# Performance work log

Hardware: AMD Instinct MI355X
Metric: run time of the kernel (lower is better)

Reference implementation:

```python
import jax, jax.numpy as jnp
import numpy as np

B, NB, T, C, H, FW, TW = 4, 64, 512, 256, 8, 8, 8
HD = C // H
SCALE = HD ** -0.5
EPS = 1e-5


def setup_inputs() -> dict:
    key = jax.random.key(0)
    ks = jax.random.split(key, 12)
    inpt = jax.random.normal(ks[0], (B, NB, T, C), jnp.float32)
    perm_n = jax.vmap(lambda k: jax.random.permutation(k, NB))(jax.random.split(ks[1], B)).astype(jnp.int32)
    perm_t = jax.vmap(lambda k: jax.random.permutation(k, T))(jax.random.split(ks[2], B)).astype(jnp.int32)
    w = lambda k, shp: (jax.random.normal(k, shp, jnp.float32) * 0.02)
    return {
        "inpt": inpt, "perm_n": perm_n, "perm_t": perm_t,
        "ln_g": jnp.ones((C,), jnp.float32), "ln_b": jnp.zeros((C,), jnp.float32),
        "Wq": w(ks[3], (C, C)), "bq": jnp.zeros((C,), jnp.float32),
        "Wk": w(ks[4], (C, C)), "bk": jnp.zeros((C,), jnp.float32),
        "Wv": w(ks[5], (C, C)), "bv": jnp.zeros((C,), jnp.float32),
        "Wp": w(ks[6], (C, C)), "bp": jnp.zeros((C,), jnp.float32),
    }


def _layernorm(x, g, b):
    m = x.mean(-1, keepdims=True)
    v = ((x - m) ** 2).mean(-1, keepdims=True)
    return (x - m) * jax.lax.rsqrt(v + EPS) * g + b


def reference(inpt, perm_n, perm_t, ln_g, ln_b, Wq, bq, Wk, bk, Wv, bv, Wp, bp):
    x = _layernorm(inpt, ln_g, ln_b)  # (B, NB, T, C)

    # per-batch shuffle: gather along N then along T
    shuffled = jax.vmap(lambda xb, pn, pt: xb[pn][:, pt])(x, perm_n, perm_t)

    # window partition -> (B*NB/FW*T/TW, FW*TW, C)
    win = shuffled.reshape(B, NB // FW, FW, T // TW, TW, C)
    win = win.transpose(0, 1, 3, 2, 4, 5).reshape(-1, FW * TW, C)

    def heads(y):  # (Bw, L, C) -> (Bw, H, L, HD)
        return y.reshape(y.shape[0], y.shape[1], H, HD).transpose(0, 2, 1, 3)

    q = heads(win @ Wq.T + bq) * SCALE
    k = heads(win @ Wk.T + bk)
    v = heads(win @ Wv.T + bv)

    attn = jax.nn.softmax(jnp.einsum('bhqd,bhkd->bhqk', q, k), axis=-1)
    o = jnp.einsum('bhqk,bhkd->bhqd', attn, v)
    o = o.transpose(0, 2, 1, 3).reshape(-1, FW * TW, C)
    o = o @ Wp.T + bp

    # window reverse -> (B, NB, T, C)
    y = o.reshape(B, NB // FW, T // TW, FW, TW, C)
    y = y.transpose(0, 1, 3, 2, 4, 5).reshape(B, NB, T, C)

    # scatter reverse == gather with inverse permutations
    inv_n = jnp.argsort(perm_n, axis=-1)
    inv_t = jnp.argsort(perm_t, axis=-1)
    unshuf = jax.vmap(lambda yb, qn, qt: yb[:, qt][qn])(y, inv_n, inv_t)

    return inpt + unshuf
```

## Files before the change

kernel.cpp:

```cpp
#include <hip/hip_runtime.h>

typedef __attribute__((ext_vector_type(4))) float f32x4;
typedef __attribute__((ext_vector_type(8))) short bf16x8;

#define EPS_ 1e-5f
#define QSC 0.25503639409729144f

#define XS 264
#define SCB 16896
#define CHUNK 7424
#define QSTR 40
#define KOFF 2560
#define PSTR 72
#define VTOFF 5120
#define VSTR 72
#define LDS_US 76288
#define LDS_BYTES (LDS_US * 2 + 256)

__device__ __forceinline__ unsigned int pack2(float a, float b) {
  union { float f; unsigned int u; } ua, ub;
  ua.f = a; ub.f = b;
  unsigned int ra = (ua.u + 0x7FFFu + ((ua.u >> 16) & 1u)) >> 16;
  unsigned int rb = (ub.u + 0x7FFFu + ((ub.u >> 16) & 1u)) & 0xFFFF0000u;
  return ra | rb;
}
__device__ __forceinline__ uint2 pack4(f32x4 v) {
  uint2 o; o.x = pack2(v[0], v[1]); o.y = pack2(v[2], v[3]); return o;
}
__device__ __forceinline__ unsigned short f2b(float f) {
  union { float f; unsigned int u; } c; c.f = f;
  return (unsigned short)((c.u + 0x7FFFu + ((c.u >> 16) & 1u)) >> 16);
}

__global__ __launch_bounds__(256) void k0_cvt(const float* __restrict__ w0,
                                              const float* __restrict__ w1,
                                              const float* __restrict__ w2,
                                              const float* __restrict__ w3,
                                              unsigned short* __restrict__ dst) {
  int idx = blockIdx.x * 256 + threadIdx.x;
  const float* s = (blockIdx.y == 0) ? w0 : (blockIdx.y == 1) ? w1 : (blockIdx.y == 2) ? w2 : w3;
  dst[blockIdx.y * 65536 + idx] = f2b(s[idx]);
}

__global__ __launch_bounds__(512, 2) void ka_fused(
    const unsigned short* __restrict__ Wall,
    const float* __restrict__ ln_g, const float* __restrict__ ln_b,
    const int* __restrict__ pn, const int* __restrict__ pt,
    const float* __restrict__ bq, const float* __restrict__ bk,
    const float* __restrict__ bv, const float* __restrict__ bp,
    const float* __restrict__ inpt, float* __restrict__ out) {
  extern __shared__ unsigned short lds[];
  int* tok_off = (int*)(lds + LDS_US);

  const int tid = threadIdx.x;
  const int wv = tid >> 6, lane = tid & 63, quad = lane >> 4, l15 = lane & 15;
  const int w = blockIdx.x;
  const int b = w >> 9, nbb = (w >> 6) & 7, tbb = w & 63;
  const f32x4 z4 = {0.f, 0.f, 0.f, 0.f};

  if (tid < 64) {
    const int n = (nbb << 3) + (tid >> 3), t = (tbb << 3) + (tid & 7);
    tok_off[tid] = (((b << 6) + pn[(b << 6) + n]) * 512 + pt[(b << 9) + t]) * 256;
  }

  {
    const int n = (nbb << 3) + wv;
    const int spn = pn[(b << 6) + n];
    const float* rowbase = inpt + (size_t)((b << 6) + spn) * 512 * 256;
    const float4 gg = ((const float4*)ln_g)[lane];
    const float4 bb = ((const float4*)ln_b)[lane];
    float4 v[8];
    #pragma unroll
    for (int i = 0; i < 8; ++i) {
      const int spt = pt[(b << 9) + (tbb << 3) + i];
      v[i] = ((const float4*)(rowbase + (size_t)spt * 256))[lane];
    }
    #pragma unroll
    for (int i = 0; i < 8; ++i) {
      float s = v[i].x + v[i].y + v[i].z + v[i].w;
      float ss = v[i].x * v[i].x + v[i].y * v[i].y + v[i].z * v[i].z + v[i].w * v[i].w;
      #pragma unroll
      for (int m = 1; m < 64; m <<= 1) { s += __shfl_xor(s, m); ss += __shfl_xor(ss, m); }
      const float mean = s * (1.0f / 256.0f);
      const float rs = rsqrtf(ss * (1.0f / 256.0f) - mean * mean + EPS_);
      ushort4 o;
      o.x = f2b((v[i].x - mean) * rs * gg.x + bb.x);
      o.y = f2b((v[i].y - mean) * rs * gg.y + bb.y);
      o.z = f2b((v[i].z - mean) * rs * gg.z + bb.z);
      o.w = f2b((v[i].w - mean) * rs * gg.w + bb.w);
      ((ushort4*)(lds + (wv * 8 + i) * XS))[lane] = o;
    }
  }
  __syncthreads();

  const unsigned short* Wq = Wall;
  const unsigned short* Wk = Wall + 65536;
  const unsigned short* Wv_ = Wall + 131072;
  const unsigned short* Wp = Wall + 196608;
  unsigned short* chunk = lds + SCB + wv * CHUNK;
  const int h = wv;

  f32x4 qa[2][4], ka_[2][4], va[4][2];
  #pragma unroll
  for (int m2 = 0; m2 < 2; ++m2)
    #pragma unroll
    for (int nt = 0; nt < 4; ++nt) { qa[m2][nt] = z4; ka_[m2][nt] = z4; }
  #pragma unroll
  for (int mt = 0; mt < 4; ++mt)
    #pragma unroll
    for (int m2 = 0; m2 < 2; ++m2) va[mt][m2] = z4;

  #pragma unroll
  for (int ks = 0; ks < 8; ++ks) {
    bf16x8 bx[4];
    #pragma unroll
    for (int nt = 0; nt < 4; ++nt)
      bx[nt] = *(const bf16x8*)(lds + (nt * 16 + l15) * XS + ks * 32 + quad * 8);
    #pragma unroll
    for (int m2 = 0; m2 < 2; ++m2) {
      const int wrow = (h * 32 + m2 * 16 + l15) * 256 + ks * 32 + quad * 8;
      bf16x8 wq8 = *(const bf16x8*)(Wq + wrow);
      bf16x8 wk8 = *(const bf16x8*)(Wk + wrow);
      bf16x8 wv8 = *(const bf16x8*)(Wv_ + wrow);
      #pragma unroll
      for (int nt = 0; nt < 4; ++nt) {
        qa[m2][nt] = __builtin_amdgcn_mfma_f32_16x16x32_bf16(wq8, bx[nt], qa[m2][nt], 0, 0, 0);
        ka_[m2][nt] = __builtin_amdgcn_mfma_f32_16x16x32_bf16(wk8, bx[nt], ka_[m2][nt], 0, 0, 0);
        va[nt][m2] = __builtin_amdgcn_mfma_f32_16x16x32_bf16(bx[nt], wv8, va[nt][m2], 0, 0, 0);
      }
    }
  }

  #pragma unroll
  for (int m2 = 0; m2 < 2; ++m2) {
    float4 bq4 = ((const float4*)(bq + h * 32 + m2 * 16))[quad];
    float4 bk4 = ((const float4*)(bk + h * 32 + m2 * 16))[quad];
    #pragma unroll
    for (int nt = 0; nt < 4; ++nt) {
      f32x4 qv, kv;
      qv[0] = (qa[m2][nt][0] + bq4.x) * QSC; kv[0] = ka_[m2][nt][0] + bk4.x;
      qv[1] = (qa[m2][nt][1] + bq4.y) * QSC; kv[1] = ka_[m2][nt][1] + bk4.y;
      qv[2] = (qa[m2][nt][2] + bq4.z) * QSC; kv[2] = ka_[m2][nt][2] + bk4.z;
      qv[3] = (qa[m2][nt][3] + bq4.w) * QSC; kv[3] = ka_[m2][nt][3] + bk4.w;
      *(uint2*)(chunk + (nt * 16 + l15) * QSTR + m2 * 16 + quad * 4) = pack4(qv);
      *(uint2*)(chunk + KOFF + (nt * 16 + l15) * QSTR + m2 * 16 + quad * 4) = pack4(kv);
    }
    const float bvv = bv[h * 32 + m2 * 16 + l15];
    #pragma unroll
    for (int mt = 0; mt < 4; ++mt) {
      f32x4 vv;
      vv[0] = va[mt][m2][0] + bvv; vv[1] = va[mt][m2][1] + bvv;
      vv[2] = va[mt][m2][2] + bvv; vv[3] = va[mt][m2][3] + bvv;
      *(uint2*)(chunk + VTOFF + (m2 * 16 + l15) * VSTR + mt * 16 + quad * 4) = pack4(vv);
    }
  }

  bf16x8 qf[4], kf[4];
  #pragma unroll
  for (int i = 0; i < 4; ++i) {
    qf[i] = *(const bf16x8*)(chunk + (i * 16 + l15) * QSTR + quad * 8);
    kf[i] = *(const bf16x8*)(chunk + KOFF + (i * 16 + l15) * QSTR + quad * 8);
  }
  f32x4 st[4][4];
  #pragma unroll
  for (int mtk = 0; mtk < 4; ++mtk)
    #pragma unroll
    for (int ntq = 0; ntq < 4; ++ntq)
      st[mtk][ntq] = __builtin_amdgcn_mfma_f32_16x16x32_bf16(kf[mtk], qf[ntq], z4, 0, 0, 0);

  float inv[4];
  #pragma unroll
  for (int ntq = 0; ntq < 4; ++ntq) {
    float tot = 0.f;
    #pragma unroll
    for (int mtk = 0; mtk < 4; ++mtk)
      #pragma unroll
      for (int r = 0; r < 4; ++r) {
        const float e = __builtin_amdgcn_exp2f(st[mtk][ntq][r]);
        st[mtk][ntq][r] = e; tot += e;
      }
    tot += __shfl_xor(tot, 16);
    tot += __shfl_xor(tot, 32);
    inv[ntq] = 1.0f / tot;
  }
  #pragma unroll
  for (int ntq = 0; ntq < 4; ++ntq)
    #pragma unroll
    for (int mtk = 0; mtk < 4; ++mtk) {
      f32x4 pv;
      pv[0] = st[mtk][ntq][0] * inv[ntq]; pv[1] = st[mtk][ntq][1] * inv[ntq];
      pv[2] = st[mtk][ntq][2] * inv[ntq]; pv[3] = st[mtk][ntq][3] * inv[ntq];
      *(uint2*)(chunk + (ntq * 16 + l15) * PSTR + mtk * 16 + quad * 4) = pack4(pv);
    }

  f32x4 oa[2][4];
  #pragma unroll
  for (int m2 = 0; m2 < 2; ++m2)
    #pragma unroll
    for (int ntq = 0; ntq < 4; ++ntq) oa[m2][ntq] = z4;
  #pragma unroll
  for (int kk = 0; kk < 2; ++kk) {
    bf16x8 pb[4], vf[2];
    #pragma unroll
    for (int ntq = 0; ntq < 4; ++ntq)
      pb[ntq] = *(const bf16x8*)(chunk + (ntq * 16 + l15) * PSTR + kk * 32 + quad * 8);
    #pragma unroll
    for (int m2 = 0; m2 < 2; ++m2)
      vf[m2] = *(const bf16x8*)(chunk + VTOFF + (m2 * 16 + l15) * VSTR + kk * 32 + quad * 8);
    #pragma unroll
    for (int m2 = 0; m2 < 2; ++m2)
      #pragma unroll
      for (int ntq = 0; ntq < 4; ++ntq)
        oa[m2][ntq] = __builtin_amdgcn_mfma_f32_16x16x32_bf16(vf[m2], pb[ntq], oa[m2][ntq], 0, 0, 0);
  }
  uint2 opk[2][4];
  #pragma unroll
  for (int m2 = 0; m2 < 2; ++m2)
    #pragma unroll
    for (int ntq = 0; ntq < 4; ++ntq) opk[m2][ntq] = pack4(oa[m2][ntq]);

  __syncthreads();
  #pragma unroll
  for (int m2 = 0; m2 < 2; ++m2)
    #pragma unroll
    for (int ntq = 0; ntq < 4; ++ntq)
      *(uint2*)(lds + (ntq * 16 + l15) * XS + h * 32 + m2 * 16 + quad * 4) = opk[m2][ntq];
  __syncthreads();

  f32x4 pacc[2][4];
  #pragma unroll
  for (int m2 = 0; m2 < 2; ++m2)
    #pragma unroll
    for (int nto = 0; nto < 4; ++nto) pacc[m2][nto] = z4;
  #pragma unroll
  for (int ks = 0; ks < 8; ++ks) {
    bf16x8 ob[4];
    #pragma unroll
    for (int nto = 0; nto < 4; ++nto)
      ob[nto] = *(const bf16x8*)(lds + (nto * 16 + l15) * XS + ks * 32 + quad * 8);
    #pragma unroll
    for (int m2 = 0; m2 < 2; ++m2) {
      bf16x8 wp8 = *(const bf16x8*)(Wp + (wv * 32 + m2 * 16 + l15) * 256 + ks * 32 + quad * 8);
      #pragma unroll
      for (int nto = 0; nto < 4; ++nto)
        pacc[m2][nto] = __builtin_amdgcn_mfma_f32_16x16x32_bf16(wp8, ob[nto], pacc[m2][nto], 0, 0, 0);
    }
  }

  #pragma unroll
  for (int m2 = 0; m2 < 2; ++m2) {
    float4 bp4 = ((const float4*)(bp + wv * 32 + m2 * 16))[quad];
    #pragma unroll
    for (int nto = 0; nto < 4; ++nto) {
      const int tok = nto * 16 + l15;
      const int off = tok_off[tok] + wv * 32 + m2 * 16 + quad * 4;
      float4 iv = *(const float4*)(inpt + off);
      float4 o;
      o.x = iv.x + pacc[m2][nto][0] + bp4.x;
      o.y = iv.y + pacc[m2][nto][1] + bp4.y;
      o.z = iv.z + pacc[m2][nto][2] + bp4.z;
      o.w = iv.w + pacc[m2][nto][3] + bp4.w;
      *(float4*)(out + off) = o;
    }
  }
}

extern "C" void kernel_launch(void* const* d_in, const int* in_sizes, int n_in,
                              void* d_out, int out_size, void* d_ws, size_t ws_size,
                              hipStream_t stream) {
  const float* inpt = (const float*)d_in[0];
  const int* perm_n = (const int*)d_in[1];
  const int* perm_t = (const int*)d_in[2];
  const float* ln_g = (const float*)d_in[3];
  const float* ln_b = (const float*)d_in[4];
  const float* Wq = (const float*)d_in[5];
  const float* bq = (const float*)d_in[6];
  const float* Wk = (const float*)d_in[7];
  const float* bk = (const float*)d_in[8];
  const float* Wv = (const float*)d_in[9];
  const float* bv = (const float*)d_in[10];
  const float* Wp = (const float*)d_in[11];
  const float* bp = (const float*)d_in[12];
  float* out = (float*)d_out;

  unsigned short* Wall = (unsigned short*)d_ws;

  (void)hipFuncSetAttribute((const void*)ka_fused,
                            hipFuncAttributeMaxDynamicSharedMemorySize, LDS_BYTES);

  k0_cvt<<<dim3(256, 4), 256, 0, stream>>>(Wq, Wk, Wv, Wp, Wall);
  ka_fused<<<2048, 512, LDS_BYTES, stream>>>(Wall, ln_g, ln_b, perm_n, perm_t,
                                             bq, bk, bv, bp, inpt, out);
}
```

Measured before the change: 438.4 us.

## Halve block to 4 waves with two heads each and XOR-swizzled LDS

Reduces the block from 512 to 256 threads, so each wave handles two attention heads and 64 output columns of the projection. Padded LDS strides are replaced by XOR swizzles, which cuts shared memory from about 150KB to 80KB per block so more blocks can fit per CU. Token offsets are now computed in registers rather than staged in LDS. The cost is more registers per wave (opk for two heads, 4x4 projection accumulators) and more serial work per wave, which could limit occupancy.

```diff
diff --git a/kernel.cpp b/kernel.cpp
--- a/kernel.cpp
+++ b/kernel.cpp
@@ -6,16 +6,16 @@
 #define EPS_ 1e-5f
 #define QSC 0.25503639409729144f
 
-#define XS 264
-#define SCB 16896
-#define CHUNK 7424
-#define QSTR 40
-#define KOFF 2560
-#define PSTR 72
-#define VTOFF 5120
-#define VSTR 72
-#define LDS_US 76288
-#define LDS_BYTES (LDS_US * 2 + 256)
+#define CBASE 16384
+#define CHUNK 6144
+#define KOFF 2048
+#define VTOFF 4096
+#define LDS_US 40960
+#define LDS_BYTES (LDS_US * 2)
+
+__device__ __forceinline__ int swzx(int r, int c) { return r * 256 + (c ^ ((r & 7) << 3)); }
+__device__ __forceinline__ int swzq(int r, int c) { return r * 32 + (c ^ (((r >> 1) & 3) << 3)); }
+__device__ __forceinline__ int swzp(int r, int c) { return r * 64 + (c ^ ((r & 7) << 3)); }
 
 __device__ __forceinline__ unsigned int pack2(float a, float b) {
   union { float f; unsigned int u; } ua, ub;
@@ -42,7 +42,7 @@
   dst[blockIdx.y * 65536 + idx] = f2b(s[idx]);
 }
 
-__global__ __launch_bounds__(512, 2) void ka_fused(
+__global__ __launch_bounds__(256, 2) void ka_fused(
     const unsigned short* __restrict__ Wall,
     const float* __restrict__ ln_g, const float* __restrict__ ln_b,
     const int* __restrict__ pn, const int* __restrict__ pt,
@@ -50,7 +50,6 @@
     const float* __restrict__ bv, const float* __restrict__ bp,
     const float* __restrict__ inpt, float* __restrict__ out) {
   extern __shared__ unsigned short lds[];
-  int* tok_off = (int*)(lds + LDS_US);
 
   const int tid = threadIdx.x;
   const int wv = tid >> 6, lane = tid & 63, quad = lane >> 4, l15 = lane & 15;
@@ -58,37 +57,36 @@
   const int b = w >> 9, nbb = (w >> 6) & 7, tbb = w & 63;
   const f32x4 z4 = {0.f, 0.f, 0.f, 0.f};
 
-  if (tid < 64) {
-    const int n = (nbb << 3) + (tid >> 3), t = (tbb << 3) + (tid & 7);
-    tok_off[tid] = (((b << 6) + pn[(b << 6) + n]) * 512 + pt[(b << 9) + t]) * 256;
-  }
-
   {
-    const int n = (nbb << 3) + wv;
-    const int spn = pn[(b << 6) + n];
-    const float* rowbase = inpt + (size_t)((b << 6) + spn) * 512 * 256;
     const float4 gg = ((const float4*)ln_g)[lane];
     const float4 bb = ((const float4*)ln_b)[lane];
-    float4 v[8];
-    #pragma unroll
-    for (int i = 0; i < 8; ++i) {
-      const int spt = pt[(b << 9) + (tbb << 3) + i];
-      v[i] = ((const float4*)(rowbase + (size_t)spt * 256))[lane];
-    }
-    #pragma unroll
-    for (int i = 0; i < 8; ++i) {
-      float s = v[i].x + v[i].y + v[i].z + v[i].w;
-      float ss = v[i].x * v[i].x + v[i].y * v[i].y + v[i].z * v[i].z + v[i].w * v[i].w;
-      #pragma unroll
-      for (int m = 1; m < 64; m <<= 1) { s += __shfl_xor(s, m); ss += __shfl_xor(ss, m); }
-      const float mean = s * (1.0f / 256.0f);
-      const float rs = rsqrtf(ss * (1.0f / 256.0f) - mean * mean + EPS_);
-      ushort4 o;
-      o.x = f2b((v[i].x - mean) * rs * gg.x + bb.x);
-      o.y = f2b((v[i].y - mean) * rs * gg.y + bb.y);
-      o.z = f2b((v[i].z - mean) * rs * gg.z + bb.z);
-      o.w = f2b((v[i].w - mean) * rs * gg.w + bb.w);
-      ((ushort4*)(lds + (wv * 8 + i) * XS))[lane] = o;
+    #pragma unroll
+    for (int ii = 0; ii < 2; ++ii) {
+      const int nloc = wv * 2 + ii;
+      const int spn = pn[(b << 6) + (nbb << 3) + nloc];
+      const float* rowbase = inpt + (size_t)((b << 6) + spn) * 512 * 256;
+      float4 v[8];
+      #pragma unroll
+      for (int i = 0; i < 8; ++i) {
+        const int spt = pt[(b << 9) + (tbb << 3) + i];
+        v[i] = ((const float4*)(rowbase + (size_t)spt * 256))[lane];
+      }
+      #pragma unroll
+      for (int i = 0; i < 8; ++i) {
+        float s = v[i].x + v[i].y + v[i].z + v[i].w;
+        float ss = v[i].x * v[i].x + v[i].y * v[i].y + v[i].z * v[i].z + v[i].w * v[i].w;
+        #pragma unroll
+        for (int m = 1; m < 64; m <<= 1) { s += __shfl_xor(s, m); ss += __shfl_xor(ss, m); }
+        const float mean = s * (1.0f / 256.0f);
+        const float rs = rsqrtf(ss * (1.0f / 256.0f) - mean * mean + EPS_);
+        ushort4 o;
+        o.x = f2b((v[i].x - mean) * rs * gg.x + bb.x);
+        o.y = f2b((v[i].y - mean) * rs * gg.y + bb.y);
+        o.z = f2b((v[i].z - mean) * rs * gg.z + bb.z);
+        o.w = f2b((v[i].w - mean) * rs * gg.w + bb.w);
+        const int row = nloc * 8 + i;
+        *(ushort4*)(lds + swzx(row, lane * 4)) = o;
+      }
     }
   }
   __syncthreads();
@@ -97,169 +95,184 @@
   const unsigned short* Wk = Wall + 65536;
   const unsigned short* Wv_ = Wall + 131072;
   const unsigned short* Wp = Wall + 196608;
-  unsigned short* chunk = lds + SCB + wv * CHUNK;
-  const int h = wv;
-
-  f32x4 qa[2][4], ka_[2][4], va[4][2];
-  #pragma unroll
-  for (int m2 = 0; m2 < 2; ++m2)
-    #pragma unroll
-    for (int nt = 0; nt < 4; ++nt) { qa[m2][nt] = z4; ka_[m2][nt] = z4; }
-  #pragma unroll
-  for (int mt = 0; mt < 4; ++mt)
-    #pragma unroll
-    for (int m2 = 0; m2 < 2; ++m2) va[mt][m2] = z4;
-
-  #pragma unroll
-  for (int ks = 0; ks < 8; ++ks) {
-    bf16x8 bx[4];
-    #pragma unroll
-    for (int nt = 0; nt < 4; ++nt)
-      bx[nt] = *(const bf16x8*)(lds + (nt * 16 + l15) * XS + ks * 32 + quad * 8);
+  unsigned short* chunk = lds + CBASE + wv * CHUNK;
+
+  uint2 opk[2][2][4];
+
+  #pragma unroll
+  for (int hh = 0; hh < 2; ++hh) {
+    const int h = (wv << 1) + hh;
+
+    f32x4 qa[2][4], ka_[2][4], va[4][2];
+    #pragma unroll
+    for (int m2 = 0; m2 < 2; ++m2)
+      #pragma unroll
+      for (int nt = 0; nt < 4; ++nt) { qa[m2][nt] = z4; ka_[m2][nt] = z4; }
+    #pragma unroll
+    for (int mt = 0; mt < 4; ++mt)
+      #pragma unroll
+      for (int m2 = 0; m2 < 2; ++m2) va[mt][m2] = z4;
+
+    #pragma unroll
+    for (int ks = 0; ks < 8; ++ks) {
+      bf16x8 bx[4];
+      #pragma unroll
+      for (int nt = 0; nt < 4; ++nt)
+        bx[nt] = *(const bf16x8*)(lds + swzx(nt * 16 + l15, ks * 32 + quad * 8));
+      #pragma unroll
+      for (int m2 = 0; m2 < 2; ++m2) {
+        const int wrow = (h * 32 + m2 * 16 + l15) * 256 + ks * 32 + quad * 8;
+        bf16x8 wq8 = *(const bf16x8*)(Wq + wrow);
+        bf16x8 wk8 = *(const bf16x8*)(Wk + wrow);
+        bf16x8 wv8 = *(const bf16x8*)(Wv_ + wrow);
+        #pragma unroll
+        for (int nt = 0; nt < 4; ++nt) {
+          qa[m2][nt] = __builtin_amdgcn_mfma_f32_16x16x32_bf16(wq8, bx[nt], qa[m2][nt], 0, 0, 0);
+          ka_[m2][nt] = __builtin_amdgcn_mfma_f32_16x16x32_bf16(wk8, bx[nt], ka_[m2][nt], 0, 0, 0);
+          va[nt][m2] = __builtin_amdgcn_mfma_f32_16x16x32_bf16(bx[nt], wv8, va[nt][m2], 0, 0, 0);
+        }
+      }
+    }
+
     #pragma unroll
     for (int m2 = 0; m2 < 2; ++m2) {
-      const int wrow = (h * 32 + m2 * 16 + l15) * 256 + ks * 32 + quad * 8;
-      bf16x8 wq8 = *(const bf16x8*)(Wq + wrow);
-      bf16x8 wk8 = *(const bf16x8*)(Wk + wrow);
-      bf16x8 wv8 = *(const bf16x8*)(Wv_ + wrow);
+      float4 bq4 = ((const float4*)(bq + h * 32 + m2 * 16))[quad];
+      float4 bk4 = ((const float4*)(bk + h * 32 + m2 * 16))[quad];
       #pragma unroll
       for (int nt = 0; nt < 4; ++nt) {
-        qa[m2][nt] = __builtin_amdgcn_mfma_f32_16x16x32_bf16(wq8, bx[nt], qa[m2][nt], 0, 0, 0);
-        ka_[m2][nt] = __builtin_amdgcn_mfma_f32_16x16x32_bf16(wk8, bx[nt], ka_[m2][nt], 0, 0, 0);
-        va[nt][m2] = __builtin_amdgcn_mfma_f32_16x16x32_bf16(bx[nt], wv8, va[nt][m2], 0, 0, 0);
-      }
-    }
-  }
-
-  #pragma unroll
-  for (int m2 = 0; m2 < 2; ++m2) {
-    float4 bq4 = ((const float4*)(bq + h * 32 + m2 * 16))[quad];
-    float4 bk4 = ((const float4*)(bk + h * 32 + m2 * 16))[quad];
-    #pragma unroll
-    for (int nt = 0; nt < 4; ++nt) {
-      f32x4 qv, kv;
-      qv[0] = (qa[m2][nt][0] + bq4.x) * QSC; kv[0] = ka_[m2][nt][0] + bk4.x;
-      qv[1] = (qa[m2][nt][1] + bq4.y) * QSC; kv[1] = ka_[m2][nt][1] + bk4.y;
-      qv[2] = (qa[m2][nt][2] + bq4.z) * QSC; kv[2] = ka_[m2][nt][2] + bk4.z;
-      qv[3] = (qa[m2][nt][3] + bq4.w) * QSC; kv[3] = ka_[m2][nt][3] + bk4.w;
-      *(uint2*)(chunk + (nt * 16 + l15) * QSTR + m2 * 16 + quad * 4) = pack4(qv);
-      *(uint2*)(chunk + KOFF + (nt * 16 + l15) * QSTR + m2 * 16 + quad * 4) = pack4(kv);
-    }
-    const float bvv = bv[h * 32 + m2 * 16 + l15];
-    #pragma unroll
-    for (int mt = 0; mt < 4; ++mt) {
-      f32x4 vv;
-      vv[0] = va[mt][m2][0] + bvv; vv[1] = va[mt][m2][1] + bvv;
-      vv[2] = va[mt][m2][2] + bvv; vv[3] = va[mt][m2][3] + bvv;
-      *(uint2*)(chunk + VTOFF + (m2 * 16 + l15) * VSTR + mt * 16 + quad * 4) = pack4(vv);
-    }
-  }
-
-  bf16x8 qf[4], kf[4];
-  #pragma unroll
-  for (int i = 0; i < 4; ++i) {
-    qf[i] = *(const bf16x8*)(chunk + (i * 16 + l15) * QSTR + quad * 8);
-    kf[i] = *(const bf16x8*)(chunk + KOFF + (i * 16 + l15) * QSTR + quad * 8);
-  }
-  f32x4 st[4][4];
-  #pragma unroll
-  for (int mtk = 0; mtk < 4; ++mtk)
+        f32x4 qv, kv;
+        qv[0] = (qa[m2][nt][0] + bq4.x) * QSC; kv[0] = ka_[m2][nt][0] + bk4.x;
+        qv[1] = (qa[m2][nt][1] + bq4.y) * QSC; kv[1] = ka_[m2][nt][1] + bk4.y;
+        qv[2] = (qa[m2][nt][2] + bq4.z) * QSC; kv[2] = ka_[m2][nt][2] + bk4.z;
+        qv[3] = (qa[m2][nt][3] + bq4.w) * QSC; kv[3] = ka_[m2][nt][3] + bk4.w;
+        const int r = nt * 16 + l15, c = m2 * 16 + quad * 4;
+        *(uint2*)(chunk + swzq(r, c)) = pack4(qv);
+        *(uint2*)(chunk + KOFF + swzq(r, c)) = pack4(kv);
+      }
+      const float bvv = bv[h * 32 + m2 * 16 + l15];
+      #pragma unroll
+      for (int mt = 0; mt < 4; ++mt) {
+        f32x4 vv;
+        vv[0] = va[mt][m2][0] + bvv; vv[1] = va[mt][m2][1] + bvv;
+        vv[2] = va[mt][m2][2] + bvv; vv[3] = va[mt][m2][3] + bvv;
+        *(uint2*)(chunk + VTOFF + swzp(m2 * 16 + l15, mt * 16 + quad * 4)) = pack4(vv);
+      }
+    }
+
+    bf16x8 qf[4], kf[4];
+    #pragma unroll
+    for (int i = 0; i < 4; ++i) {
+      qf[i] = *(const bf16x8*)(chunk + swzq(i * 16 + l15, quad * 8));
+      kf[i] = *(const bf16x8*)(chunk + KOFF + swzq(i * 16 + l15, quad * 8));
+    }
+    f32x4 st[4][4];
+    #pragma unroll
+    for (int mtk = 0; mtk < 4; ++mtk)
+      #pragma unroll
+      for (int ntq = 0; ntq < 4; ++ntq)
+        st[mtk][ntq] = __builtin_amdgcn_mfma_f32_16x16x32_bf16(kf[mtk], qf[ntq], z4, 0, 0, 0);
+
+    float inv[4];
+    #pragma unroll
+    for (int ntq = 0; ntq < 4; ++ntq) {
+      float tot = 0.f;
+      #pragma unroll
+      for (int mtk = 0; mtk < 4; ++mtk)
+        #pragma unroll
+        for (int r = 0; r < 4; ++r) {
+          const float e = __builtin_amdgcn_exp2f(st[mtk][ntq][r]);
+          st[mtk][ntq][r] = e; tot += e;
+        }
+      tot += __shfl_xor(tot, 16);
+      tot += __shfl_xor(tot, 32);
+      inv[ntq] = 1.0f / tot;
+    }
     #pragma unroll
     for (int ntq = 0; ntq < 4; ++ntq)
-      st[mtk][ntq] = __builtin_amdgcn_mfma_f32_16x16x32_bf16(kf[mtk], qf[ntq], z4, 0, 0, 0);
-
-  float inv[4];
-  #pragma unroll
-  for (int ntq = 0; ntq < 4; ++ntq) {
-    float tot = 0.f;
-    #pragma unroll
-    for (int mtk = 0; mtk < 4; ++mtk)
-      #pragma unroll
-      for (int r = 0; r < 4; ++r) {
-        const float e = __builtin_amdgcn_exp2f(st[mtk][ntq][r]);
-        st[mtk][ntq][r] = e; tot += e;
-      }
-    tot += __shfl_xor(tot, 16);
-    tot += __shfl_xor(tot, 32);
-    inv[ntq] = 1.0f / tot;
-  }
-  #pragma unroll
-  for (int ntq = 0; ntq < 4; ++ntq)
-    #pragma unroll
-    for (int mtk = 0; mtk < 4; ++mtk) {
-      f32x4 pv;
-      pv[0] = st[mtk][ntq][0] * inv[ntq]; pv[1] = st[mtk][ntq][1] * inv[ntq];
-      pv[2] = st[mtk][ntq][2] * inv[ntq]; pv[3] = st[mtk][ntq][3] * inv[ntq];
-      *(uint2*)(chunk + (ntq * 16 + l15) * PSTR + mtk * 16 + quad * 4) = pack4(pv);
-    }
-
-  f32x4 oa[2][4];
-  #pragma unroll
-  for (int m2 = 0; m2 < 2; ++m2)
-    #pragma unroll
-    for (int ntq = 0; ntq < 4; ++ntq) oa[m2][ntq] = z4;
-  #pragma unroll
-  for (int kk = 0; kk < 2; ++kk) {
-    bf16x8 pb[4], vf[2];
-    #pragma unroll
-    for (int ntq = 0; ntq < 4; ++ntq)
-      pb[ntq] = *(const bf16x8*)(chunk + (ntq * 16 + l15) * PSTR + kk * 32 + quad * 8);
+      #pragma unroll
+      for (int mtk = 0; mtk < 4; ++mtk) {
+        f32x4 pv;
+        pv[0] = st[mtk][ntq][0] * inv[ntq]; pv[1] = st[mtk][ntq][1] * inv[ntq];
+        pv[2] = st[mtk][ntq][2] * inv[ntq]; pv[3] = st[mtk][ntq][3] * inv[ntq];
+        *(uint2*)(chunk + swzp(ntq * 16 + l15, mtk * 16 + quad * 4)) = pack4(pv);
+      }
+
+    f32x4 oa[2][4];
     #pragma unroll
     for (int m2 = 0; m2 < 2; ++m2)
-      vf[m2] = *(const bf16x8*)(chunk + VTOFF + (m2 * 16 + l15) * VSTR + kk * 32 + quad * 8);
+      #pragma unroll
+      for (int ntq = 0; ntq < 4; ++ntq) oa[m2][ntq] = z4;
+    #pragma unroll
+    for (int kk = 0; kk < 2; ++kk) {
+      bf16x8 pb[4], vf[2];
+      #pragma unroll
+      for (int ntq = 0; ntq < 4; ++ntq)
+        pb[ntq] = *(const bf16x8*)(chunk + swzp(ntq * 16 + l15, kk * 32 + quad * 8));
+      #pragma unroll
+      for (int m2 = 0; m2 < 2; ++m2)
+        vf[m2] = *(const bf16x8*)(chunk + VTOFF + swzp(m2 * 16 + l15, kk * 32 + quad * 8));
+      #pragma unroll
+      for (int m2 = 0; m2 < 2; ++m2)
+        #pragma unroll
+        for (int ntq = 0; ntq < 4; ++ntq)
+          oa[m2][ntq] = __builtin_amdgcn_mfma_f32_16x16x32_bf16(vf[m2], pb[ntq], oa[m2][ntq], 0, 0, 0);
+    }
     #pragma unroll
     for (int m2 = 0; m2 < 2; ++m2)
       #pragma unroll
+      for (int ntq = 0; ntq < 4; ++ntq) opk[hh][m2][ntq] = pack4(oa[m2][ntq]);
+  }
+
+  __syncthreads();
+  #pragma unroll
+  for (int hh = 0; hh < 2; ++hh)
+    #pragma unroll
+    for (int m2 = 0; m2 < 2; ++m2)
+      #pragma unroll
       for (int ntq = 0; ntq < 4; ++ntq)
-        oa[m2][ntq] = __builtin_amdgcn_mfma_f32_16x16x32_bf16(vf[m2], pb[ntq], oa[m2][ntq], 0, 0, 0);
-  }
-  uint2 opk[2][4];
-  #pragma unroll
-  for (int m2 = 0; m2 < 2; ++m2)
-    #pragma unroll
-    for (int ntq = 0; ntq < 4; ++ntq) opk[m2][ntq] = pack4(oa[m2][ntq]);
-
+        *(uint2*)(lds + swzx(ntq * 16 + l15, ((wv * 2 + hh) * 32 + m2 * 16 + quad * 4))) =
+            opk[hh][m2][ntq];
   __syncthreads();
-  #pragma unroll
-  for (int m2 = 0; m2 < 2; ++m2)
-    #pragma unroll
-    for (int ntq = 0; ntq < 4; ++ntq)
-      *(uint2*)(lds + (ntq * 16 + l15) * XS + h * 32 + m2 * 16 + quad * 4) = opk[m2][ntq];
-  __syncthreads();
-
-  f32x4 pacc[2][4];
-  #pragma unroll
-  for (int m2 = 0; m2 < 2; ++m2)
-    #pragma unroll
-    for (int nto = 0; nto < 4; ++nto) pacc[m2][nto] = z4;
+
+  f32x4 pacc[4][4];
+  #pragma unroll
+  for (int m4 = 0; m4 < 4; ++m4)
+    #pragma unroll
+    for (int nto = 0; nto < 4; ++nto) pacc[m4][nto] = z4;
   #pragma unroll
   for (int ks = 0; ks < 8; ++ks) {
     bf16x8 ob[4];
     #pragma unroll
     for (int nto = 0; nto < 4; ++nto)
-      ob[nto] = *(const bf16x8*)(lds + (nto * 16 + l15) * XS + ks * 32 + quad * 8);
-    #pragma unroll
-    for (int m2 = 0; m2 < 2; ++m2) {
-      bf16x8 wp8 = *(const bf16x8*)(Wp + (wv * 32 + m2 * 16 + l15) * 256 + ks * 32 + quad * 8);
+      ob[nto] = *(const bf16x8*)(lds + swzx(nto * 16 + l15, ks * 32 + quad * 8));
+    #pragma unroll
+    for (int m4 = 0; m4 < 4; ++m4) {
+      bf16x8 wp8 = *(const bf16x8*)(Wp + (wv * 64 + m4 * 16 + l15) * 256 + ks * 32 + quad * 8);
       #pragma unroll
       for (int nto = 0; nto < 4; ++nto)
-        pacc[m2][nto] = __builtin_amdgcn_mfma_f32_16x16x32_bf16(wp8, ob[nto], pacc[m2][nto], 0, 0, 0);
-    }
-  }
-
-  #pragma unroll
-  for (int m2 = 0; m2 < 2; ++m2) {
-    float4 bp4 = ((const float4*)(bp + wv * 32 + m2 * 16))[quad];
+        pacc[m4][nto] = __builtin_amdgcn_mfma_f32_16x16x32_bf16(wp8, ob[nto], pacc[m4][nto], 0, 0, 0);
+    }
+  }
+
+  int toff[4];
+  #pragma unroll
+  for (int nto = 0; nto < 4; ++nto) {
+    const int tok = nto * 16 + l15;
+    const int n = (nbb << 3) + (tok >> 3), t = (tbb << 3) + (tok & 7);
+    toff[nto] = (((b << 6) + pn[(b << 6) + n]) * 512 + pt[(b << 9) + t]) * 256;
+  }
+  #pragma unroll
+  for (int m4 = 0; m4 < 4; ++m4) {
+    float4 bp4 = ((const float4*)(bp + wv * 64 + m4 * 16))[quad];
     #pragma unroll
     for (int nto = 0; nto < 4; ++nto) {
-      const int tok = nto * 16 + l15;
-      const int off = tok_off[tok] + wv * 32 + m2 * 16 + quad * 4;
+      const int off = toff[nto] + wv * 64 + m4 * 16 + quad * 4;
       float4 iv = *(const float4*)(inpt + off);
       float4 o;
-      o.x = iv.x + pacc[m2][nto][0] + bp4.x;
-      o.y = iv.y + pacc[m2][nto][1] + bp4.y;
-      o.z = iv.z + pacc[m2][nto][2] + bp4.z;
-      o.w = iv.w + pacc[m2][nto][3] + bp4.w;
+      o.x = iv.x + pacc[m4][nto][0] + bp4.x;
+      o.y = iv.y + pacc[m4][nto][1] + bp4.y;
+      o.z = iv.z + pacc[m4][nto][2] + bp4.z;
+      o.w = iv.w + pacc[m4][nto][3] + bp4.w;
       *(float4*)(out + off) = o;
     }
   }
@@ -289,6 +302,6 @@
                             hipFuncAttributeMaxDynamicSharedMemorySize, LDS_BYTES);
 
   k0_cvt<<<dim3(256, 4), 256, 0, stream>>>(Wq, Wk, Wv, Wp, Wall);
-  ka_fused<<<2048, 512, LDS_BYTES, stream>>>(Wall, ln_g, ln_b, perm_n, perm_t,
+  ka_fused<<<2048, 256, LDS_BYTES, stream>>>(Wall, ln_g, ln_b, perm_n, perm_t,
                                              bq, bk, bv, bp, inpt, out);
 }
```

New measurement: 456.5 us. +4.1%, slower.
